# Optimization experiments

Hardware: AMD Instinct MI355X
Metric: run time of the kernel (lower is better)

Reference implementation:

```python
import jax, jax.numpy as jnp
from jax import lax
import numpy as np

B, C, L, K = 8, 512, 2048, 3
CQ = C // 8


def setup_inputs() -> dict:
    key = jax.random.key(0)
    k1, k2, k3, k4 = jax.random.split(key, 4)
    scale = 0.05
    return {
        "x": jax.random.normal(k1, (B, C, L), dtype=jnp.float32),
        "Wq": jax.random.normal(k2, (CQ, C, K), dtype=jnp.float32) * scale,
        "Wk": jax.random.normal(k3, (CQ, C, K), dtype=jnp.float32) * scale,
        "Wv": jax.random.normal(k4, (C, C, K), dtype=jnp.float32) * scale,
        "gamma": jnp.ones((1,), dtype=jnp.float32),
    }


def _conv1d(x, w):
    # x: [B, Cin, L], w: [Cout, Cin, K]; 'same' padding = (K-1)//2 on both sides
    pad = (w.shape[-1] - 1) // 2
    return lax.conv_general_dilated(
        x, w, window_strides=(1,), padding=[(pad, pad)],
        dimension_numbers=("NCH", "OIH", "NCH"))


def reference(x, Wq, Wk, Wv, gamma):
    q = _conv1d(x, Wq)  # [B, C/8, L]
    k = _conv1d(x, Wk)  # [B, C/8, L]
    v = _conv1d(x, Wv)  # [B, C, L]
    # scores[b, i, j] = sum_c q[b, c, i] * k[b, c, j]  (q^T k)
    scores = jnp.einsum("bci,bcj->bij", q, k)
    # softmax over dim=1 (the query/i axis) — non-standard axis
    beta = jax.nn.softmax(scores, axis=1)  # [B, L, L]
    out = gamma * jnp.einsum("bcl,blj->bcj", v, beta)  # [B, C, L]
    return out
```

## Files before the change

### kernel.cpp

```cpp
#include <hip/hip_runtime.h>
#include <cstddef>
#include <math.h>

#define L_DIM 2048
#define C_DIM 512
#define CQ_DIM 64
#define B_DIM 8
#define LOG2E 1.44269504088896340736f

typedef _Float16 f16x8 __attribute__((ext_vector_type(8)));
typedef __fp16 fp16x2_t __attribute__((ext_vector_type(2)));
typedef float f32x4 __attribute__((ext_vector_type(4)));

typedef __attribute__((address_space(3))) unsigned int u32_lds;
typedef __attribute__((address_space(1))) const unsigned int u32_glob;

__device__ __forceinline__ unsigned short f2h(float f) {
    union { _Float16 h; unsigned short u; } v;
    v.h = (_Float16)f;
    return v.u;
}

__device__ __forceinline__ unsigned p2u(float a, float b) {
    union { fp16x2_t h; unsigned u; } v;
    v.h = __builtin_amdgcn_cvt_pkrtz(a, b);
    return v.u;
}

__device__ __forceinline__ void gll16(const unsigned short* g, unsigned short* l) {
    __builtin_amdgcn_global_load_lds((u32_glob*)(const void*)g,
                                     (u32_lds*)(void*)l, 16, 0, 0);
}


__global__ __launch_bounds__(256) void prep_w(const float* __restrict__ Wq,
                                              const float* __restrict__ Wk,
                                              const float* __restrict__ Wv,
                                              unsigned short* __restrict__ Wh) {
    const int idx = blockIdx.x * 256 + threadIdx.x;
    const int ci = idx & 511;
    const int co = (idx >> 9) % 640;
    const int t  = idx / (640 * 512);
    float w;
    if (co < 64)       w = Wq[(size_t)co * 1536 + ci * 3 + t];
    else if (co < 128) w = Wk[(size_t)(co - 64) * 1536 + ci * 3 + t];
    else               w = Wv[(size_t)(co - 128) * 1536 + ci * 3 + t];
    Wh[idx] = f2h(w);
}

__global__ __launch_bounds__(256) void prep_x(const float* __restrict__ x,
                                              unsigned short* __restrict__ xT) {
    const int l0  = blockIdx.x * 64;
    const int ci0 = blockIdx.y * 64;
    const int b   = blockIdx.z;

    __shared__ float xs[64][68];
    const int tid = threadIdx.x;
    const float* xb = x + ((size_t)b * C_DIM + ci0) * L_DIM;

    for (int idx = tid; idx < 64 * 16; idx += 256) {
        int ci = idx >> 4, lq = idx & 15;
        *(float4*)&xs[ci][lq * 4] = *(const float4*)&xb[(size_t)ci * L_DIM + l0 + lq * 4];
    }
    __syncthreads();

    unsigned short* ob = xT + ((size_t)b * L_DIM + l0) * C_DIM + ci0;
    for (int idx = tid; idx < 64 * 8; idx += 256) {
        int l = idx >> 3, c8 = idx & 7;
        ushort4 r0, r1;
        r0.x = f2h(xs[c8 * 8 + 0][l]); r0.y = f2h(xs[c8 * 8 + 1][l]);
        r0.z = f2h(xs[c8 * 8 + 2][l]); r0.w = f2h(xs[c8 * 8 + 3][l]);
        r1.x = f2h(xs[c8 * 8 + 4][l]); r1.y = f2h(xs[c8 * 8 + 5][l]);
        r1.z = f2h(xs[c8 * 8 + 6][l]); r1.w = f2h(xs[c8 * 8 + 7][l]);
        *(ushort4*)&ob[(size_t)l * C_DIM + c8 * 8] = r0;
        *(ushort4*)&ob[(size_t)l * C_DIM + c8 * 8 + 4] = r1;
    }
}

__global__ __launch_bounds__(256) void conv_all(const unsigned short* __restrict__ Wh,
                                                const unsigned short* __restrict__ xT,
                                                unsigned short* __restrict__ qT,
                                                unsigned short* __restrict__ kT,
                                                unsigned short* __restrict__ vB) {
    const int l0  = blockIdx.x * 128;
    const int co0 = blockIdx.y * 64;
    const int b   = blockIdx.z;

    __shared__ unsigned short As[3][64][40];
    __shared__ unsigned short Bs[130][40];

    const int tid  = threadIdx.x;
    const int lane = tid & 63, w = tid >> 6;
    const int ln15 = lane & 15, quad = lane >> 4;

    const int co_w = (w & 1) * 32;
    const int l_w  = (w >> 1) * 64;

    const unsigned short* xb = xT + (size_t)b * L_DIM * C_DIM;

    f32x4 acc[2][4] = {};

    for (int ci0 = 0; ci0 < C_DIM; ci0 += 32) {
        __syncthreads();
        for (int idx = tid; idx < 768; idx += 256) {
            int t = idx >> 8, co = (idx >> 2) & 63, c8 = idx & 3;
            *(float4*)&As[t][co][c8 * 8] =
                *(const float4*)&Wh[(((size_t)t * 640) + co0 + co) * C_DIM + ci0 + c8 * 8];
        }
        for (int idx = tid; idx < 520; idx += 256) {
            int la = idx >> 2, c8 = idx & 3;
            int l = l0 - 1 + la;
            float4 vx = {0.f, 0.f, 0.f, 0.f};
            if (l >= 0 && l < L_DIM)
                vx = *(const float4*)&xb[(size_t)l * C_DIM + ci0 + c8 * 8];
            *(float4*)&Bs[la][c8 * 8] = vx;
        }
        __syncthreads();

#pragma unroll
        for (int t = 0; t < 3; t++) {
            f16x8 a[2], bfr[4];
#pragma unroll
            for (int ct = 0; ct < 2; ct++)
                a[ct] = *(const f16x8*)&As[t][co_w + ct * 16 + ln15][quad * 8];
#pragma unroll
            for (int lt = 0; lt < 4; lt++)
                bfr[lt] = *(const f16x8*)&Bs[l_w + lt * 16 + ln15 + t][quad * 8];
#pragma unroll
            for (int ct = 0; ct < 2; ct++)
#pragma unroll
                for (int lt = 0; lt < 4; lt++)
                    acc[ct][lt] = __builtin_amdgcn_mfma_f32_16x16x32_f16(a[ct], bfr[lt], acc[ct][lt], 0, 0, 0);
        }
    }

    if (co0 < 128) {
        const float qs = (co0 == 0) ? LOG2E : 1.0f;
        unsigned short* dst = (co0 == 0 ? qT : kT) + (size_t)b * L_DIM * CQ_DIM;
#pragma unroll
        for (int ct = 0; ct < 2; ct++)
#pragma unroll
            for (int lt = 0; lt < 4; lt++) {
                const int l = l0 + l_w + lt * 16 + ln15;
                const int c = co_w + ct * 16 + quad * 4;
                ushort4 r;
                r.x = f2h(acc[ct][lt][0] * qs); r.y = f2h(acc[ct][lt][1] * qs);
                r.z = f2h(acc[ct][lt][2] * qs); r.w = f2h(acc[ct][lt][3] * qs);
                const size_t off = (size_t)(l >> 4) * 1024 + (c >> 5) * 512
                                 + (((c >> 3) & 3) * 16 + (l & 15)) * 8 + (c & 7);
                *(ushort4*)&dst[off] = r;
            }
    } else {
        unsigned short* dst = vB + (size_t)b * C_DIM * L_DIM;
#pragma unroll
        for (int ct = 0; ct < 2; ct++)
#pragma unroll
            for (int lt = 0; lt < 4; lt++) {
                const int l = l0 + l_w + lt * 16 + ln15;
                const size_t ibase = ((size_t)(l >> 6) * 32) * 1024 + ((l >> 5) & 1) * 512
                                   + (((l >> 3) & 3) * 16) * 8 + (l & 7);
#pragma unroll
                for (int r = 0; r < 4; r++) {
                    const int vco = (co0 - 128) + co_w + ct * 16 + quad * 4 + r;
                    dst[ibase + (size_t)(vco >> 4) * 1024 + (vco & 15) * 8] = f2h(acc[ct][lt][r]);
                }
            }
    }
}

__global__ __launch_bounds__(256) void stat_k(const unsigned short* __restrict__ qT,
                                              const unsigned short* __restrict__ kT,
                                              float* __restrict__ pstat) {
    const int ich = blockIdx.x;
    const int j0  = blockIdx.y * 64;
    const int b   = blockIdx.z;

    const int tid = threadIdx.x;
    const int lane = tid & 63, w = tid >> 6;
    const int ln15 = lane & 15, quad = lane >> 4;
    const int sj = w * 16;
    const int lane8 = lane * 8;

    const unsigned short* qb = qT + (size_t)b * L_DIM * CQ_DIM;
    const unsigned short* kb = kT + (size_t)b * L_DIM * CQ_DIM;

    f16x8 kfr[2];
#pragma unroll
    for (int cc = 0; cc < 2; cc++)
        kfr[cc] = *(const f16x8*)&kb[(size_t)((j0 + sj) >> 4) * 1024 + cc * 512 + lane8];

    float m_run = -1e30f, l_run = 0.f;

    for (int t = 0; t < 4; t++) {
        const int ib = ich * 16 + t * 4;

        f32x4 sacc[4] = {};
#pragma unroll
        for (int cc = 0; cc < 2; cc++) {
#pragma unroll
            for (int it = 0; it < 4; it++) {
                const f16x8 afr = *(const f16x8*)&qb[(size_t)(ib + it) * 1024 + cc * 512 + lane8];
                sacc[it] = __builtin_amdgcn_mfma_f32_16x16x32_f16(afr, kfr[cc], sacc[it], 0, 0, 0);
            }
        }

        float bm = -1e30f;
#pragma unroll
        for (int it = 0; it < 4; it++)
#pragma unroll
            for (int r = 0; r < 4; r++)
                bm = fmaxf(bm, sacc[it][r]);
        bm = fmaxf(bm, __shfl_xor(bm, 16, 64));
        bm = fmaxf(bm, __shfl_xor(bm, 32, 64));
        const float m_new = fmaxf(m_run, bm);
        const float alpha = exp2f(m_run - m_new);

        float lsum = 0.f;
#pragma unroll
        for (int it = 0; it < 4; it++) {
            float p0 = exp2f(sacc[it][0] - m_new);
            float p1 = exp2f(sacc[it][1] - m_new);
            float p2 = exp2f(sacc[it][2] - m_new);
            float p3 = exp2f(sacc[it][3] - m_new);
            lsum += (p0 + p1) + (p2 + p3);
        }
        lsum += __shfl_xor(lsum, 16, 64);
        lsum += __shfl_xor(lsum, 32, 64);
        l_run = l_run * alpha + lsum;
        m_run = m_new;
    }

    if (quad == 0) {
        const int j = j0 + sj + ln15;
        float* pm = pstat;
        float* pl = pstat + 8 * 8 * 2048;
        pm[((size_t)ich * 8 + b) * 2048 + j] = m_run;
        pl[((size_t)ich * 8 + b) * 2048 + j] = l_run;
    }
}

__global__ __launch_bounds__(256) void pv2(const unsigned short* __restrict__ qT,
                                           const unsigned short* __restrict__ kT,
                                           const unsigned short* __restrict__ vB,
                                           const float* __restrict__ pstat,
                                           const float* __restrict__ gamma,
                                           float* __restrict__ out) {
    const int j0  = blockIdx.x * 64;
    const int co0 = blockIdx.y * 128;
    const int b   = blockIdx.z;

    __shared__ __align__(16) unsigned short qbuf[2][4096];
    __shared__ __align__(16) unsigned short vbuf[2][8192];
    __shared__ unsigned short pps[64 * 68];
    __shared__ float mj_s[64];
    __shared__ float il_s[64];

    const int tid = threadIdx.x;
    const int lane = tid & 63, w = tid >> 6;
    const int ln15 = lane & 15, quad = lane >> 4;
    const int lane8 = lane * 8;

    const unsigned short* qb = qT + (size_t)b * L_DIM * CQ_DIM;
    const unsigned short* kb = kT + (size_t)b * L_DIM * CQ_DIM;
    const unsigned short* vb = vB + (size_t)b * C_DIM * L_DIM;

    const int sj  = w * 16;
    const int wco = w * 32;

    if (tid < 64) {
        const int j = j0 + tid;
        const float* pm = pstat;
        const float* pl = pstat + 8 * 8 * 2048;
        float m = -1e30f;
        float pmv[8];
#pragma unroll
        for (int c = 0; c < 8; c++) {
            pmv[c] = pm[((size_t)c * 8 + b) * 2048 + j];
            m = fmaxf(m, pmv[c]);
        }
        float l = 0.f;
#pragma unroll
        for (int c = 0; c < 8; c++)
            l = fmaf(pl[((size_t)c * 8 + b) * 2048 + j], exp2f(pmv[c] - m), l);
        mj_s[tid] = m;
        il_s[tid] = gamma[0] / l;
    }

    f16x8 kfr[2];
#pragma unroll
    for (int cc = 0; cc < 2; cc++)
        kfr[cc] = *(const f16x8*)&kb[(size_t)((j0 + sj) >> 4) * 1024 + cc * 512 + lane8];

    {
        const unsigned short* vsrc = vb + (size_t)(co0 >> 4) * 1024;
#pragma unroll
        for (int s = 0; s < 2; s++)
            gll16(qb + (w * 2 + s) * 512 + lane8, &qbuf[0][(w * 2 + s) * 512]);
#pragma unroll
        for (int s = 0; s < 4; s++)
            gll16(vsrc + (w * 4 + s) * 512 + lane8, &vbuf[0][(w * 4 + s) * 512]);
    }
    __syncthreads();

    const float m_lane = mj_s[sj + ln15];
    float inv[4];
#pragma unroll
    for (int bb = 0; bb < 4; bb++)
        inv[bb] = il_s[bb * 16 + ln15];

    f32x4 oacc[2][4] = {};
    int cur = 0;

    for (int i0 = 0; i0 < L_DIM; i0 += 64) {
        const int i1 = i0 + 64;
        if (i1 < L_DIM) {
            const unsigned short* qsrc = qb + (size_t)(i1 >> 4) * 1024;
            const unsigned short* vsrc = vb + ((size_t)(i1 >> 6) * 32 + (co0 >> 4)) * 1024;
            const int nxt = cur ^ 1;
#pragma unroll
            for (int s = 0; s < 2; s++)
                gll16(qsrc + (w * 2 + s) * 512 + lane8, &qbuf[nxt][(w * 2 + s) * 512]);
#pragma unroll
            for (int s = 0; s < 4; s++)
                gll16(vsrc + (w * 4 + s) * 512 + lane8, &vbuf[nxt][(w * 4 + s) * 512]);
        }

        f32x4 sacc[4] = {};
        __builtin_amdgcn_s_setprio(1);
#pragma unroll
        for (int cc = 0; cc < 2; cc++) {
#pragma unroll
            for (int it = 0; it < 4; it++) {
                const f16x8 afr = *(const f16x8*)&qbuf[cur][(it * 2 + cc) * 512 + lane8];
                sacc[it] = __builtin_amdgcn_mfma_f32_16x16x32_f16(afr, kfr[cc], sacc[it], 0, 0, 0);
            }
        }
        __builtin_amdgcn_s_setprio(0);

        const int j = sj + ln15;
#pragma unroll
        for (int it = 0; it < 4; it++) {
            float p0 = exp2f(sacc[it][0] - m_lane);
            float p1 = exp2f(sacc[it][1] - m_lane);
            float p2 = exp2f(sacc[it][2] - m_lane);
            float p3 = exp2f(sacc[it][3] - m_lane);
            uint2 u;
            u.x = p2u(p0, p1);
            u.y = p2u(p2, p3);
            *(uint2*)&pps[j * 68 + it * 16 + quad * 4] = u;
        }

        asm volatile("s_waitcnt lgkmcnt(0)" ::: "memory");
        __builtin_amdgcn_s_barrier();
        __builtin_amdgcn_sched_barrier(0);

        __builtin_amdgcn_s_setprio(1);
#pragma unroll
        for (int cc = 0; cc < 2; cc++) {
            f16x8 afr[2], bfr[4];
#pragma unroll
            for (int t = 0; t < 2; t++)
                afr[t] = *(const f16x8*)&vbuf[cur][((w * 2 + t) * 2 + cc) * 512 + lane8];
#pragma unroll
            for (int t = 0; t < 4; t++)
                bfr[t] = *(const f16x8*)&pps[(t * 16 + ln15) * 68 + cc * 32 + quad * 8];
#pragma unroll
            for (int a = 0; a < 2; a++)
#pragma unroll
                for (int bb = 0; bb < 4; bb++)
                    oacc[a][bb] = __builtin_amdgcn_mfma_f32_16x16x32_f16(afr[a], bfr[bb], oacc[a][bb], 0, 0, 0);
        }
        __builtin_amdgcn_s_setprio(0);

        __syncthreads();
        cur ^= 1;
    }

#pragma unroll
    for (int a = 0; a < 2; a++)
#pragma unroll
        for (int r = 0; r < 4; r++) {
            const int co = co0 + wco + a * 16 + quad * 4 + r;
            float* ob = out + ((size_t)b * C_DIM + co) * L_DIM + j0;
#pragma unroll
            for (int bb = 0; bb < 4; bb++)
                ob[bb * 16 + ln15] = oacc[a][bb][r] * inv[bb];
        }
}

extern "C" void kernel_launch(void* const* d_in, const int* in_sizes, int n_in,
                              void* d_out, int out_size, void* d_ws, size_t ws_size,
                              hipStream_t stream) {
    const float* x     = (const float*)d_in[0];
    const float* Wq    = (const float*)d_in[1];
    const float* Wk    = (const float*)d_in[2];
    const float* Wv    = (const float*)d_in[3];
    const float* gamma = (const float*)d_in[4];
    float* out = (float*)d_out;

    unsigned short* ws_h = (unsigned short*)d_ws;
    unsigned short* qT = ws_h;
    unsigned short* kT = qT + 1048576;
    unsigned short* vB = kT + 1048576;
    unsigned short* xT = vB + 8388608;
    unsigned short* Wh = xT + 8388608;
    float* pstat = (float*)xT;

    prep_w  <<<3840, 256, 0, stream>>>(Wq, Wk, Wv, Wh);
    prep_x  <<<dim3(32, 8, 8), 256, 0, stream>>>(x, xT);
    conv_all<<<dim3(16, 10, 8), 256, 0, stream>>>(Wh, xT, qT, kT, vB);
    stat_k  <<<dim3(8, 32, 8), 256, 0, stream>>>(qT, kT, pstat);
    pv2     <<<dim3(32, 4, 8), 256, 0, stream>>>(qT, kT, vB, pstat, gamma, out);
}
```

Baseline: 250.9 us.

## Pipeline conv_all with triple-buffered direct global-to-LDS loads and swizzled layout

Rewrites the conv_all main loop so it uses a triple-buffered LDS ring filled by asynchronous global-to-LDS 16-byte loads (gll16). The next ci-slice is prefetched while MFMAs run on the current one, synchronised with explicit vmcnt waits and one barrier per stage. The x tile uses an XOR-style row rotation swizzle, and boundary rows are clamped and then zeroed in LDS. The goal is to hide global-load latency and remove register-staged copies and a double barrier, at the cost of fragile hand-tuned waitcnt counts and padding logic.

```diff
diff --git a/kernel.cpp b/kernel.cpp
--- a/kernel.cpp
+++ b/kernel.cpp
@@ -86,54 +86,81 @@
     const int co0 = blockIdx.y * 64;
     const int b   = blockIdx.z;
 
-    __shared__ unsigned short As[3][64][40];
-    __shared__ unsigned short Bs[130][40];
+    __shared__ __align__(16) unsigned short sbuf[3][21 * 512];
 
     const int tid  = threadIdx.x;
     const int lane = tid & 63, w = tid >> 6;
     const int ln15 = lane & 15, quad = lane >> 4;
-
-    const int co_w = (w & 1) * 32;
-    const int l_w  = (w >> 1) * 64;
+    const int cw  = w & 1;
+    const int lw_ = (w >> 1) * 64;
 
     const unsigned short* xb = xT + (size_t)b * L_DIM * C_DIM;
 
+    const int apre = ln15 * 512 + quad * 8;
+    const int bpre = (ln15 - 2 * quad) & 15;
+    const int bci  = quad * 8;
+
     f32x4 acc[2][4] = {};
 
-    for (int ci0 = 0; ci0 < C_DIM; ci0 += 32) {
-        __syncthreads();
-        for (int idx = tid; idx < 768; idx += 256) {
-            int t = idx >> 8, co = (idx >> 2) & 63, c8 = idx & 3;
-            *(float4*)&As[t][co][c8 * 8] =
-                *(const float4*)&Wh[(((size_t)t * 640) + co0 + co) * C_DIM + ci0 + c8 * 8];
-        }
-        for (int idx = tid; idx < 520; idx += 256) {
-            int la = idx >> 2, c8 = idx & 3;
-            int l = l0 - 1 + la;
-            float4 vx = {0.f, 0.f, 0.f, 0.f};
-            if (l >= 0 && l < L_DIM)
-                vx = *(const float4*)&xb[(size_t)l * C_DIM + ci0 + c8 * 8];
-            *(float4*)&Bs[la][c8 * 8] = vx;
-        }
-        __syncthreads();
-
+#define CONV_STAGE(ci_, bi_)                                                              \
+    _Pragma("unroll")                                                                     \
+    for (int k = 0; k < 6; k++) {                                                         \
+        const int c = w + k * 4;                                                          \
+        if (c < 21) {                                                                     \
+            if (c < 12) {                                                                 \
+                const unsigned short* src = Wh                                            \
+                    + ((size_t)(c >> 2) * 640 + co0 + ((c >> 1) & 1) * 32 + (c & 1) * 16) * 512 \
+                    + apre + (ci_);                                                       \
+                gll16(src, &sbuf[bi_][c * 512]);                                          \
+            } else {                                                                      \
+                int rr = l0 - 1 + (c - 12) * 16 + bpre;                                   \
+                rr = rr < 0 ? 0 : (rr > 2047 ? 2047 : rr);                                \
+                gll16(xb + (size_t)rr * 512 + bci + (ci_), &sbuf[bi_][c * 512]);          \
+            }                                                                             \
+        }                                                                                 \
+    }
+
+    CONV_STAGE(0, 0);
+    __builtin_amdgcn_sched_barrier(0);
+
+    for (int s = 0; s < 16; s++) {
+        if (s + 1 < 16) { CONV_STAGE((s + 1) * 32, (s + 1) % 3); }
+        __builtin_amdgcn_sched_barrier(0);
+        if (s + 1 < 16) {
+            if (w == 0) asm volatile("s_waitcnt vmcnt(6)" ::: "memory");
+            else        asm volatile("s_waitcnt vmcnt(5)" ::: "memory");
+        } else {
+            asm volatile("s_waitcnt vmcnt(0)" ::: "memory");
+        }
+        __builtin_amdgcn_sched_barrier(0);
+        if (l0 == 0 && w == 0 && lane < 4)
+            *(f32x4*)&sbuf[s % 3][12 * 512 + lane * 144] = (f32x4){0.f, 0.f, 0.f, 0.f};
+        if (l0 == 1920 && w == 0 && lane < 4)
+            *(f32x4*)&sbuf[s % 3][20 * 512 + 8 + lane * 144] = (f32x4){0.f, 0.f, 0.f, 0.f};
+        asm volatile("s_waitcnt lgkmcnt(0)" ::: "memory");
+        __builtin_amdgcn_s_barrier();
+        __builtin_amdgcn_sched_barrier(0);
+
+        const unsigned short* Sb = sbuf[s % 3];
+        __builtin_amdgcn_s_setprio(1);
 #pragma unroll
         for (int t = 0; t < 3; t++) {
-            f16x8 a[2], bfr[4];
-#pragma unroll
-            for (int ct = 0; ct < 2; ct++)
-                a[ct] = *(const f16x8*)&As[t][co_w + ct * 16 + ln15][quad * 8];
-#pragma unroll
-            for (int lt = 0; lt < 4; lt++)
-                bfr[lt] = *(const f16x8*)&Bs[l_w + lt * 16 + ln15 + t][quad * 8];
-#pragma unroll
-            for (int ct = 0; ct < 2; ct++)
-#pragma unroll
-                for (int lt = 0; lt < 4; lt++)
-                    acc[ct][lt] = __builtin_amdgcn_mfma_f32_16x16x32_f16(a[ct], bfr[lt], acc[ct][lt], 0, 0, 0);
-        }
-    }
-
+            const f16x8 a0 = *(const f16x8*)&Sb[(size_t)(t * 4 + cw * 2 + 0) * 512 + lane * 8];
+            const f16x8 a1 = *(const f16x8*)&Sb[(size_t)(t * 4 + cw * 2 + 1) * 512 + lane * 8];
+#pragma unroll
+            for (int lt = 0; lt < 4; lt++) {
+                const int rbase = lw_ + lt * 16 + ln15 + t;
+                const f16x8 bf = *(const f16x8*)&Sb[(size_t)(12 + (rbase >> 4)) * 512
+                                   + (quad * 16 + (((rbase & 15) + 2 * quad) & 15)) * 8];
+                acc[0][lt] = __builtin_amdgcn_mfma_f32_16x16x32_f16(a0, bf, acc[0][lt], 0, 0, 0);
+                acc[1][lt] = __builtin_amdgcn_mfma_f32_16x16x32_f16(a1, bf, acc[1][lt], 0, 0, 0);
+            }
+        }
+        __builtin_amdgcn_s_setprio(0);
+    }
+
+    const int co_w = cw * 32;
+    const int l_w  = lw_;
     if (co0 < 128) {
         const float qs = (co0 == 0) ? LOG2E : 1.0f;
         unsigned short* dst = (co0 == 0 ? qT : kT) + (size_t)b * L_DIM * CQ_DIM;
```

Measured after the change: 255.2 us. About the same (+1.7%).
